# Optimization experiments

Measured on AMD Instinct MI355X. Metric: run time of the kernel, lower is better.

## Reference

```python
import jax, jax.numpy as jnp
import numpy as np

B, H, S, Q = 32768, 896, 448, 256  # batch, hidden, split=hidden//2, quantisation


def setup_inputs() -> dict:
    key = jax.random.key(0)
    ks = jax.random.split(key, 16)
    sc = 0.02
    return {
        'prev_y': jax.random.uniform(ks[0], (B, 2), jnp.float32) * 2.0 - 1.0,
        'prev_hidden': jax.random.normal(ks[1], (B, H), jnp.float32),
        'current_coarse': jax.random.uniform(ks[2], (B, 1), jnp.float32) * 2.0 - 1.0,
        'W_R': jax.random.normal(ks[3], (H, 3 * H), jnp.float32) * sc,
        'W_Ic': jax.random.normal(ks[4], (2, 3 * S), jnp.float32) * sc,
        'W_If': jax.random.normal(ks[5], (3, 3 * S), jnp.float32) * sc,
        'W_O1': jax.random.normal(ks[6], (S, S), jnp.float32) * sc,
        'b_O1': jnp.zeros((S,), jnp.float32),
        'W_O2': jax.random.normal(ks[7], (S, Q), jnp.float32) * sc,
        'b_O2': jnp.zeros((Q,), jnp.float32),
        'W_O3': jax.random.normal(ks[8], (S, S), jnp.float32) * sc,
        'b_O3': jnp.zeros((S,), jnp.float32),
        'W_O4': jax.random.normal(ks[9], (S, Q), jnp.float32) * sc,
        'b_O4': jnp.zeros((Q,), jnp.float32),
        'bias_u': jnp.zeros((H,), jnp.float32),
        'bias_r': jnp.zeros((H,), jnp.float32),
        'bias_e': jnp.zeros((H,), jnp.float32),
    }


def reference(prev_y, prev_hidden, current_coarse, W_R, W_Ic, W_If,
              W_O1, b_O1, W_O2, b_O2, W_O3, b_O3, W_O4, b_O4,
              bias_u, bias_r, bias_e):
    # recurrent projection of previous hidden state: [B, 3H]
    R_u, R_r, R_e = jnp.split(prev_hidden @ W_R, 3, axis=1)
    # coarse-half input projection from (prev_coarse, prev_fine): [B, 3S]
    I_cu, I_cr, I_ce = jnp.split(prev_y @ W_Ic, 3, axis=1)
    # fine-half input projection from (prev_coarse, prev_fine, current_coarse): [B, 3S]
    fine_in = jnp.concatenate([prev_y, current_coarse], axis=1)
    I_fu, I_fr, I_fe = jnp.split(fine_in @ W_If, 3, axis=1)
    I_u = jnp.concatenate([I_cu, I_fu], axis=1)
    I_r = jnp.concatenate([I_cr, I_fr], axis=1)
    I_e = jnp.concatenate([I_ce, I_fe], axis=1)
    u = jax.nn.sigmoid(R_u + I_u + bias_u)
    r = jax.nn.sigmoid(R_r + I_r + bias_r)
    e = jnp.tanh(r * R_e + I_e + bias_e)
    hidden = u * prev_hidden + (1.0 - u) * e
    h_c, h_f = jnp.split(hidden, 2, axis=1)
    out_coarse = jax.nn.relu(h_c @ W_O1 + b_O1) @ W_O2 + b_O2
    out_fine = jax.nn.relu(h_f @ W_O3 + b_O3) @ W_O4 + b_O4
    return out_coarse, out_fine, hidden
```

## Files before the change

kernel.cpp:

```cpp
#include <hip/hip_runtime.h>


typedef unsigned short u16;
typedef unsigned int u32;
typedef __attribute__((ext_vector_type(8))) short bf16x8;
typedef __attribute__((ext_vector_type(4))) float f32x4;

#define GAS __attribute__((address_space(1)))
#define LAS __attribute__((address_space(3)))

__device__ __forceinline__ u16 f2b(float f) {
  union { float f; u32 i; } v; v.f = f;
  return (u16)((v.i + 0x7fffu + ((v.i >> 16) & 1u)) >> 16);
}

__device__ __forceinline__ void gl_lds(const u16* g, u16* l) {
  __builtin_amdgcn_global_load_lds((const GAS void*)g, (LAS void*)l, 16, 0, 0);
}

__global__ void cvt_f32_bf16(const float* __restrict__ in, u16* __restrict__ outp) {
  const size_t i = ((size_t)blockIdx.x * 256 + threadIdx.x) * 4;
  const float4 v = *(const float4*)&in[i];
  ushort4 o;
  o.x = f2b(v.x); o.y = f2b(v.y); o.z = f2b(v.z); o.w = f2b(v.w);
  *(ushort4*)&outp[i] = o;
}

__device__ __forceinline__ void transpose_body(const float* __restrict__ in,
                                               u16* __restrict__ outp,
                                               int R, int C, int c0, int r0) {
  __shared__ u16 t[32][33];
  const int x = threadIdx.x, y = threadIdx.y;
  #pragma unroll
  for (int i = 0; i < 32; i += 8)
    t[y + i][x] = f2b(in[(size_t)(r0 + y + i) * C + (c0 + x)]);
  __syncthreads();
  #pragma unroll
  for (int i = 0; i < 32; i += 8)
    outp[(size_t)(c0 + y + i) * R + (r0 + x)] = t[x][y + i];
}

__global__ void transpose_f32_bf16(const float* __restrict__ in, u16* __restrict__ outp,
                                   int R, int C) {
  transpose_body(in, outp, R, C, blockIdx.x * 32, blockIdx.y * 32);
}

__global__ void transpose_wo(const float* __restrict__ w1, const float* __restrict__ w2,
                             const float* __restrict__ w3, const float* __restrict__ w4,
                             u16* __restrict__ o1, u16* __restrict__ o2,
                             u16* __restrict__ o3, u16* __restrict__ o4) {
  const int z = blockIdx.z;
  const float* in = (z == 0) ? w1 : (z == 1) ? w2 : (z == 2) ? w3 : w4;
  u16* outp = (z == 0) ? o1 : (z == 1) ? o2 : (z == 2) ? o3 : o4;
  const int C = (z & 1) ? 256 : 448;
  const int c0 = blockIdx.x * 32;
  if (c0 >= C) return;
  transpose_body(in, outp, 448, C, c0, blockIdx.y * 32);
}

__device__ __forceinline__ void gemm_tile_k(const u16* __restrict__ A, int lda,
                                            const u16* __restrict__ BT, int ldb,
                                            int K, u16* Al, u16* Bl,
                                            int wave, int lane, f32x4 (&acc)[4][4]) {
  const int wm = wave & 1, wn = wave >> 1;
  const int q = lane >> 4, l16 = lane & 15;
  const int qs = q ^ ((l16 >> 1) & 3);
  const int sr = lane >> 2;
  const int sc = ((lane & 3) ^ ((lane >> 3) & 3)) * 8;
  for (int k0 = 0; k0 < K; k0 += 32) {
    #pragma unroll
    for (int i = 0; i < 2; ++i) {
      const int rr = wave * 32 + i * 16;
      gl_lds(A + (size_t)(rr + sr) * lda + (k0 + sc), &Al[rr * 32]);
      gl_lds(BT + (size_t)(rr + sr) * ldb + (k0 + sc), &Bl[rr * 32]);
    }
    __syncthreads();
    bf16x8 af[4], bfr[4];
    #pragma unroll
    for (int t = 0; t < 4; ++t) {
      af[t]  = *(const bf16x8*)&Al[(wm * 64 + t * 16 + l16) * 32 + qs * 8];
      bfr[t] = *(const bf16x8*)&Bl[(wn * 64 + t * 16 + l16) * 32 + qs * 8];
    }
    #pragma unroll
    for (int mt = 0; mt < 4; ++mt)
      #pragma unroll
      for (int nt = 0; nt < 4; ++nt)
        acc[mt][nt] = __builtin_amdgcn_mfma_f32_16x16x32_bf16(af[mt], bfr[nt],
                                                              acc[mt][nt], 0, 0, 0);
    __syncthreads();
  }
}

__device__ __forceinline__ void zero_acc(f32x4 (&acc)[4][4]) {
  const f32x4 z = {0.f, 0.f, 0.f, 0.f};
  #pragma unroll
  for (int mt = 0; mt < 4; ++mt)
    #pragma unroll
    for (int nt = 0; nt < 4; ++nt)
      acc[mt][nt] = z;
}

__global__ __launch_bounds__(1024, 4)
void gate_kernel(const u16* __restrict__ phb, const u16* __restrict__ wrt,
                 const float* __restrict__ phf,
                 const float* __restrict__ y2, const float* __restrict__ cc,
                 const float* __restrict__ wic, const float* __restrict__ wif,
                 const float* __restrict__ bu, const float* __restrict__ br,
                 const float* __restrict__ be,
                 float* __restrict__ houtf, u16* __restrict__ hb) {
  __shared__ u16 Sl[3][16384];
  __shared__ float rowy[3 * 128];
  const int tid = threadIdx.x;
  const int lane = tid & 63, wave = tid >> 6;
  const int f = blockIdx.x;
  const int xcd = f & 7, l = f >> 3;
  const int m0 = (xcd * 32 + l / 7) * 128;
  const int j0 = (l % 7) * 128;
  if (tid < 128) {
    const int r = m0 + tid;
    rowy[tid]       = y2[2 * r];
    rowy[128 + tid] = y2[2 * r + 1];
    rowy[256 + tid] = cc[r];
    asm volatile("s_waitcnt lgkmcnt(0)" ::: "memory");
  }
  const int wm = wave & 3, wn = wave >> 2;
  const int q = lane >> 4, l16 = lane & 15;
  const int qs = q ^ ((l16 >> 1) & 3);
  const int sr = lane >> 2;
  const int sc = ((lane & 3) ^ ((lane >> 3) & 3)) * 8;

  const int u0 = 2 * wave, u1 = u0 + 1;
  const u16* g0; const u16* g1; int lo0, lo1;
  if (u0 < 8) { g0 = phb + (size_t)(m0 + u0 * 16 + sr) * 896 + sc; lo0 = u0 * 512; }
  else { const int nn = u0 - 8, jj = nn / 3, s = nn % 3;
         g0 = wrt + (size_t)(s * 896 + j0 + jj * 16 + sr) * 896 + sc;
         lo0 = 4096 + nn * 512; }
  if (u1 < 8) { g1 = phb + (size_t)(m0 + u1 * 16 + sr) * 896 + sc; lo1 = u1 * 512; }
  else { const int nn = u1 - 8, jj = nn / 3, s = nn % 3;
         g1 = wrt + (size_t)(s * 896 + j0 + jj * 16 + sr) * 896 + sc;
         lo1 = 4096 + nn * 512; }

  f32x4 acc[2][3][2];
  {
    const f32x4 z = {0.f, 0.f, 0.f, 0.f};
    #pragma unroll
    for (int a = 0; a < 2; ++a)
      #pragma unroll
      for (int s = 0; s < 3; ++s)
        #pragma unroll
        for (int m = 0; m < 2; ++m)
          acc[a][s][m] = z;
  }

  auto stage = [&](int t_) {
    const int b_ = t_ % 3;
    const int k_ = t_ * 32;
    gl_lds(g0 + k_, &Sl[b_][lo0]);
    gl_lds(g1 + k_, &Sl[b_][lo1]);
  };

  stage(0);
  stage(1);
  for (int t = 0; t < 28; ++t) {
    if (t < 27) asm volatile("s_waitcnt vmcnt(2)" ::: "memory");
    else        asm volatile("s_waitcnt vmcnt(0)" ::: "memory");
    __builtin_amdgcn_s_barrier();
    __builtin_amdgcn_sched_barrier(0);
    const u16* Sb = Sl[t % 3];
    bf16x8 af[2];
    #pragma unroll
    for (int mt = 0; mt < 2; ++mt)
      af[mt] = *(const bf16x8*)&Sb[(wm * 32 + mt * 16 + l16) * 32 + qs * 8];
    #pragma unroll
    for (int jj2 = 0; jj2 < 2; ++jj2)
      #pragma unroll
      for (int s = 0; s < 3; ++s) {
        const int nn = (2 * wn + jj2) * 3 + s;
        const bf16x8 bf_ = *(const bf16x8*)&Sb[4096 + nn * 512 + l16 * 32 + qs * 8];
        #pragma unroll
        for (int mt = 0; mt < 2; ++mt)
          acc[jj2][s][mt] = __builtin_amdgcn_mfma_f32_16x16x32_bf16(
              af[mt], bf_, acc[jj2][s][mt], 0, 0, 0);
      }
    if (t + 2 < 28) stage(t + 2);
  }

  #pragma unroll
  for (int jj2 = 0; jj2 < 2; ++jj2) {
    const int j = j0 + (2 * wn + jj2) * 16 + l16;
    float wu0, wu1, wu2, wr0, wr1, wr2, we0, we1, we2;
    if (j < 448) {
      wu0 = wic[j];       wu1 = wic[1344 + j];       wu2 = 0.f;
      wr0 = wic[448 + j]; wr1 = wic[1792 + j];       wr2 = 0.f;
      we0 = wic[896 + j]; we1 = wic[2240 + j];       we2 = 0.f;
    } else {
      const int jf = j - 448;
      wu0 = wif[jf];       wu1 = wif[1344 + jf]; wu2 = wif[2688 + jf];
      wr0 = wif[448 + jf]; wr1 = wif[1792 + jf]; wr2 = wif[3136 + jf];
      we0 = wif[896 + jf]; we1 = wif[2240 + jf]; we2 = wif[3584 + jf];
    }
    const float bju = bu[j], bjr = br[j], bje = be[j];
    #pragma unroll
    for (int mt = 0; mt < 2; ++mt) {
      const int rl = wm * 32 + mt * 16 + q * 4;
      #pragma unroll
      for (int i = 0; i < 4; ++i) {
        const float y0 = rowy[rl + i], y1 = rowy[128 + rl + i], yc = rowy[256 + rl + i];
        const float gu = acc[jj2][0][mt][i] + y0 * wu0 + y1 * wu1 + yc * wu2 + bju;
        const float gr = acc[jj2][1][mt][i] + y0 * wr0 + y1 * wr1 + yc * wr2 + bjr;
        const float uu = 1.f / (1.f + __expf(-gu));
        const float rg = 1.f / (1.f + __expf(-gr));
        const float ev = tanhf(rg * acc[jj2][2][mt][i] +
                               y0 * we0 + y1 * we1 + yc * we2 + bje);
        const size_t grow = (size_t)(m0 + rl + i);
        const float phv = phf[grow * 896 + j];
        const float h = uu * phv + (1.f - uu) * ev;
        houtf[grow * 896 + j] = h;
        hb[grow * 896 + j] = f2b(h);
      }
    }
  }
}

__global__ __launch_bounds__(256, 2)
void stage1_kernel(const u16* __restrict__ hb, const u16* __restrict__ w1t,
                   const u16* __restrict__ w3t, const float* __restrict__ b1,
                   const float* __restrict__ b3, u16* __restrict__ tc,
                   u16* __restrict__ tf) {
  __shared__ u16 Al[128 * 32];
  __shared__ u16 Bl[128 * 32];
  const int tid = threadIdx.x, lane = tid & 63, wave = tid >> 6;
  const int f = blockIdx.x;
  const int xcd = f & 7, l = f >> 3;
  const int mz = xcd * 64 + (l >> 2);
  const int z = mz >> 8;
  const int m0 = (mz & 255) * 128, n0 = (l & 3) * 128;
  const u16* A = hb + (size_t)m0 * 896 + z * 448;
  const u16* BT = (z ? w3t : w1t) + (size_t)n0 * 448;
  const float* bias = z ? b3 : b1;
  u16* T = z ? tf : tc;
  const int wm = wave & 1, wn = wave >> 1, q = lane >> 4, l16 = lane & 15;
  f32x4 acc[4][4];
  zero_acc(acc);
  gemm_tile_k(A, 896, BT, 448, 448, Al, Bl, wave, lane, acc);
  #pragma unroll
  for (int nt = 0; nt < 4; ++nt) {
    const int j = n0 + wn * 64 + nt * 16 + l16;
    if (j < 448) {
      const float bv = bias[j];
      #pragma unroll
      for (int mt = 0; mt < 4; ++mt)
        #pragma unroll
        for (int i = 0; i < 4; ++i) {
          const size_t row = (size_t)(m0 + wm * 64 + mt * 16 + q * 4 + i);
          T[row * 448 + j] = f2b(fmaxf(acc[mt][nt][i] + bv, 0.f));
        }
    }
  }
}

__global__ __launch_bounds__(256, 2)
void stage2_kernel(const u16* __restrict__ tc, const u16* __restrict__ tf,
                   const u16* __restrict__ w2t, const u16* __restrict__ w4t,
                   const float* __restrict__ b2_, const float* __restrict__ b4,
                   float* __restrict__ out) {
  __shared__ u16 Al[128 * 32];
  __shared__ u16 Bl[128 * 32];
  const int tid = threadIdx.x, lane = tid & 63, wave = tid >> 6;
  const int f = blockIdx.x;
  const int xcd = f & 7, l = f >> 3;
  const int mz = xcd * 64 + (l >> 1);
  const int z = mz >> 8;
  const int m0 = (mz & 255) * 128, n0 = (l & 1) * 128;
  const u16* A = (z ? tf : tc) + (size_t)m0 * 448;
  const u16* BT = (z ? w4t : w2t) + (size_t)n0 * 448;
  const float* bias = z ? b4 : b2_;
  float* O = out + (size_t)z * 32768 * 256;
  const int wm = wave & 1, wn = wave >> 1, q = lane >> 4, l16 = lane & 15;
  f32x4 acc[4][4];
  zero_acc(acc);
  gemm_tile_k(A, 448, BT, 448, 448, Al, Bl, wave, lane, acc);
  #pragma unroll
  for (int nt = 0; nt < 4; ++nt) {
    const int j = n0 + wn * 64 + nt * 16 + l16;
    const float bv = bias[j];
    #pragma unroll
    for (int mt = 0; mt < 4; ++mt)
      #pragma unroll
      for (int i = 0; i < 4; ++i) {
        const size_t row = (size_t)(m0 + wm * 64 + mt * 16 + q * 4 + i);
        O[row * 256 + j] = acc[mt][nt][i] + bv;
      }
  }
}

extern "C" void kernel_launch(void* const* d_in, const int* in_sizes, int n_in,
                              void* d_out, int out_size, void* d_ws, size_t ws_size,
                              hipStream_t stream) {
  const float* y2   = (const float*)d_in[0];
  const float* ph   = (const float*)d_in[1];
  const float* cc   = (const float*)d_in[2];
  const float* W_R  = (const float*)d_in[3];
  const float* W_Ic = (const float*)d_in[4];
  const float* W_If = (const float*)d_in[5];
  const float* W_O1 = (const float*)d_in[6];
  const float* b_O1 = (const float*)d_in[7];
  const float* W_O2 = (const float*)d_in[8];
  const float* b_O2 = (const float*)d_in[9];
  const float* W_O3 = (const float*)d_in[10];
  const float* b_O3 = (const float*)d_in[11];
  const float* W_O4 = (const float*)d_in[12];
  const float* b_O4 = (const float*)d_in[13];
  const float* bu   = (const float*)d_in[14];
  const float* br   = (const float*)d_in[15];
  const float* be   = (const float*)d_in[16];
  float* out = (float*)d_out;
  u16* ws  = (u16*)d_ws;

  u16* WRT = ws;
  u16* W1T = WRT + (size_t)2688 * 896;
  u16* W2T = W1T + 448 * 448;
  u16* W3T = W2T + 256 * 448;
  u16* W4T = W3T + 448 * 448;
  u16* phb = W4T + 256 * 448;
  u16* hb  = phb + (size_t)32768 * 896;
  u16* Tc  = phb;
  u16* Tf  = phb + (size_t)32768 * 448;
  float* hidf = out + (size_t)2 * 32768 * 256;

  dim3 tb(32, 8);
  cvt_f32_bf16<<<28672, 256, 0, stream>>>(ph, phb);
  transpose_f32_bf16<<<dim3(2688 / 32, 896 / 32), tb, 0, stream>>>(W_R, WRT, 896, 2688);
  transpose_wo<<<dim3(14, 14, 4), tb, 0, stream>>>(W_O1, W_O2, W_O3, W_O4,
                                                   W1T, W2T, W3T, W4T);

  gate_kernel<<<1792, 1024, 0, stream>>>(phb, WRT, ph, y2, cc, W_Ic, W_If,
                                         bu, br, be, hidf, hb);
  stage1_kernel<<<2048, 256, 0, stream>>>(hb, W1T, W3T, b_O1, b_O3, Tc, Tf);
  stage2_kernel<<<1024, 256, 0, stream>>>(Tc, Tf, W2T, W4T, b_O2, b_O4, out);
}
```

Measured before the change: 632.7 us.

## Load A fragments directly from global, enlarge gate tile, triple-buffer MLP GEMMs

The gate kernel now covers 256 rows per block instead of 128, with half as many blocks. Each wave loads its A (hidden-state) fragments straight from global memory into registers, and only the W_R tiles are staged in LDS, at K-steps of 64 with triple buffering. The two MLP stage kernels replace their synchronous double-barrier GEMM loop with the same scheme: A read directly from global memory and B triple-buffered in LDS through async global-to-LDS loads. This is meant to cut LDS traffic and barriers, and to give more MFMA work per staged byte. The cost is uncoalesced direct global A loads and higher register pressure, with occupancy bounds changed to 3.

```diff
diff --git a/kernel.cpp b/kernel.cpp
--- a/kernel.cpp
+++ b/kernel.cpp
@@ -58,49 +58,7 @@
   transpose_body(in, outp, 448, C, c0, blockIdx.y * 32);
 }
 
-__device__ __forceinline__ void gemm_tile_k(const u16* __restrict__ A, int lda,
-                                            const u16* __restrict__ BT, int ldb,
-                                            int K, u16* Al, u16* Bl,
-                                            int wave, int lane, f32x4 (&acc)[4][4]) {
-  const int wm = wave & 1, wn = wave >> 1;
-  const int q = lane >> 4, l16 = lane & 15;
-  const int qs = q ^ ((l16 >> 1) & 3);
-  const int sr = lane >> 2;
-  const int sc = ((lane & 3) ^ ((lane >> 3) & 3)) * 8;
-  for (int k0 = 0; k0 < K; k0 += 32) {
-    #pragma unroll
-    for (int i = 0; i < 2; ++i) {
-      const int rr = wave * 32 + i * 16;
-      gl_lds(A + (size_t)(rr + sr) * lda + (k0 + sc), &Al[rr * 32]);
-      gl_lds(BT + (size_t)(rr + sr) * ldb + (k0 + sc), &Bl[rr * 32]);
-    }
-    __syncthreads();
-    bf16x8 af[4], bfr[4];
-    #pragma unroll
-    for (int t = 0; t < 4; ++t) {
-      af[t]  = *(const bf16x8*)&Al[(wm * 64 + t * 16 + l16) * 32 + qs * 8];
-      bfr[t] = *(const bf16x8*)&Bl[(wn * 64 + t * 16 + l16) * 32 + qs * 8];
-    }
-    #pragma unroll
-    for (int mt = 0; mt < 4; ++mt)
-      #pragma unroll
-      for (int nt = 0; nt < 4; ++nt)
-        acc[mt][nt] = __builtin_amdgcn_mfma_f32_16x16x32_bf16(af[mt], bfr[nt],
-                                                              acc[mt][nt], 0, 0, 0);
-    __syncthreads();
-  }
-}
-
-__device__ __forceinline__ void zero_acc(f32x4 (&acc)[4][4]) {
-  const f32x4 z = {0.f, 0.f, 0.f, 0.f};
-  #pragma unroll
-  for (int mt = 0; mt < 4; ++mt)
-    #pragma unroll
-    for (int nt = 0; nt < 4; ++nt)
-      acc[mt][nt] = z;
-}
-
-__global__ __launch_bounds__(1024, 4)
+__global__ __launch_bounds__(1024, 3)
 void gate_kernel(const u16* __restrict__ phb, const u16* __restrict__ wrt,
                  const float* __restrict__ phf,
                  const float* __restrict__ y2, const float* __restrict__ cc,
@@ -108,19 +66,19 @@
                  const float* __restrict__ bu, const float* __restrict__ br,
                  const float* __restrict__ be,
                  float* __restrict__ houtf, u16* __restrict__ hb) {
-  __shared__ u16 Sl[3][16384];
-  __shared__ float rowy[3 * 128];
+  __shared__ u16 Bl[3][24576];
+  __shared__ float rowy[3 * 256];
   const int tid = threadIdx.x;
   const int lane = tid & 63, wave = tid >> 6;
   const int f = blockIdx.x;
   const int xcd = f & 7, l = f >> 3;
-  const int m0 = (xcd * 32 + l / 7) * 128;
+  const int m0 = (xcd * 16 + l / 7) * 256;
   const int j0 = (l % 7) * 128;
-  if (tid < 128) {
+  if (tid < 256) {
     const int r = m0 + tid;
     rowy[tid]       = y2[2 * r];
-    rowy[128 + tid] = y2[2 * r + 1];
-    rowy[256 + tid] = cc[r];
+    rowy[256 + tid] = y2[2 * r + 1];
+    rowy[512 + tid] = cc[r];
     asm volatile("s_waitcnt lgkmcnt(0)" ::: "memory");
   }
   const int wm = wave & 3, wn = wave >> 2;
@@ -129,18 +87,18 @@
   const int sr = lane >> 2;
   const int sc = ((lane & 3) ^ ((lane >> 3) & 3)) * 8;
 
-  const int u0 = 2 * wave, u1 = u0 + 1;
-  const u16* g0; const u16* g1; int lo0, lo1;
-  if (u0 < 8) { g0 = phb + (size_t)(m0 + u0 * 16 + sr) * 896 + sc; lo0 = u0 * 512; }
-  else { const int nn = u0 - 8, jj = nn / 3, s = nn % 3;
-         g0 = wrt + (size_t)(s * 896 + j0 + jj * 16 + sr) * 896 + sc;
-         lo0 = 4096 + nn * 512; }
-  if (u1 < 8) { g1 = phb + (size_t)(m0 + u1 * 16 + sr) * 896 + sc; lo1 = u1 * 512; }
-  else { const int nn = u1 - 8, jj = nn / 3, s = nn % 3;
-         g1 = wrt + (size_t)(s * 896 + j0 + jj * 16 + sr) * 896 + sc;
-         lo1 = 4096 + nn * 512; }
-
-  f32x4 acc[2][3][2];
+  const u16* ag = phb + (size_t)(m0 + wm * 64 + l16) * 896 + q * 8;
+
+  const u16* gs[3]; int lo[3];
+  #pragma unroll
+  for (int i = 0; i < 3; ++i) {
+    const int u = 3 * wave + i, nn = u >> 1, kh = u & 1;
+    const int s = nn % 3, jj = nn / 3;
+    gs[i] = wrt + (size_t)(s * 896 + j0 + jj * 16 + sr) * 896 + (kh * 32 + sc);
+    lo[i] = u * 512;
+  }
+
+  f32x4 acc[2][3][4];
   {
     const f32x4 z = {0.f, 0.f, 0.f, 0.f};
     #pragma unroll
@@ -148,41 +106,48 @@
       #pragma unroll
       for (int s = 0; s < 3; ++s)
         #pragma unroll
-        for (int m = 0; m < 2; ++m)
+        for (int m = 0; m < 4; ++m)
           acc[a][s][m] = z;
   }
 
   auto stage = [&](int t_) {
-    const int b_ = t_ % 3;
-    const int k_ = t_ * 32;
-    gl_lds(g0 + k_, &Sl[b_][lo0]);
-    gl_lds(g1 + k_, &Sl[b_][lo1]);
+    u16* base = &Bl[t_ % 3][0];
+    const int koff = t_ * 64;
+    #pragma unroll
+    for (int i = 0; i < 3; ++i) gl_lds(gs[i] + koff, base + lo[i]);
   };
 
-  stage(0);
-  stage(1);
-  for (int t = 0; t < 28; ++t) {
-    if (t < 27) asm volatile("s_waitcnt vmcnt(2)" ::: "memory");
-    else        asm volatile("s_waitcnt vmcnt(0)" ::: "memory");
+  stage(0); stage(1);
+  for (int t = 0; t < 14; ++t) {
+    if (t == 0) asm volatile("s_waitcnt vmcnt(3)" ::: "memory");
+    else        asm volatile("s_waitcnt vmcnt(11)" ::: "memory");
     __builtin_amdgcn_s_barrier();
     __builtin_amdgcn_sched_barrier(0);
-    const u16* Sb = Sl[t % 3];
-    bf16x8 af[2];
-    #pragma unroll
-    for (int mt = 0; mt < 2; ++mt)
-      af[mt] = *(const bf16x8*)&Sb[(wm * 32 + mt * 16 + l16) * 32 + qs * 8];
-    #pragma unroll
-    for (int jj2 = 0; jj2 < 2; ++jj2)
-      #pragma unroll
-      for (int s = 0; s < 3; ++s) {
-        const int nn = (2 * wn + jj2) * 3 + s;
-        const bf16x8 bf_ = *(const bf16x8*)&Sb[4096 + nn * 512 + l16 * 32 + qs * 8];
-        #pragma unroll
-        for (int mt = 0; mt < 2; ++mt)
-          acc[jj2][s][mt] = __builtin_amdgcn_mfma_f32_16x16x32_bf16(
-              af[mt], bf_, acc[jj2][s][mt], 0, 0, 0);
+    bf16x8 af[2][4];
+    #pragma unroll
+    for (int kh = 0; kh < 2; ++kh)
+      #pragma unroll
+      for (int mt = 0; mt < 4; ++mt)
+        af[kh][mt] = *(const bf16x8*)(ag + (size_t)mt * 16 * 896 + t * 64 + kh * 32);
+    stage(t + 2 < 13 ? t + 2 : 13);
+    const u16* Sb = &Bl[t % 3][0];
+    #pragma unroll
+    for (int kh = 0; kh < 2; ++kh)
+      #pragma unroll
+      for (int jj2 = 0; jj2 < 2; ++jj2) {
+        bf16x8 bf_[3];
+        #pragma unroll
+        for (int s = 0; s < 3; ++s) {
+          const int nn = (2 * wn + jj2) * 3 + s;
+          bf_[s] = *(const bf16x8*)&Sb[nn * 1024 + kh * 512 + l16 * 32 + qs * 8];
+        }
+        #pragma unroll
+        for (int s = 0; s < 3; ++s)
+          #pragma unroll
+          for (int mt = 0; mt < 4; ++mt)
+            acc[jj2][s][mt] = __builtin_amdgcn_mfma_f32_16x16x32_bf16(
+                af[kh][mt], bf_[s], acc[jj2][s][mt], 0, 0, 0);
       }
-    if (t + 2 < 28) stage(t + 2);
   }
 
   #pragma unroll
@@ -201,11 +166,11 @@
     }
     const float bju = bu[j], bjr = br[j], bje = be[j];
     #pragma unroll
-    for (int mt = 0; mt < 2; ++mt) {
-      const int rl = wm * 32 + mt * 16 + q * 4;
+    for (int mt = 0; mt < 4; ++mt) {
+      const int rl = wm * 64 + mt * 16 + q * 4;
       #pragma unroll
       for (int i = 0; i < 4; ++i) {
-        const float y0 = rowy[rl + i], y1 = rowy[128 + rl + i], yc = rowy[256 + rl + i];
+        const float y0 = rowy[rl + i], y1 = rowy[256 + rl + i], yc = rowy[512 + rl + i];
         const float gu = acc[jj2][0][mt][i] + y0 * wu0 + y1 * wu1 + yc * wu2 + bju;
         const float gr = acc[jj2][1][mt][i] + y0 * wr0 + y1 * wr1 + yc * wr2 + bjr;
         const float uu = 1.f / (1.f + __expf(-gu));
@@ -222,13 +187,74 @@
   }
 }
 
-__global__ __launch_bounds__(256, 2)
+__device__ __forceinline__ void mlp_gemm(const u16* __restrict__ A, int lda,
+                                         const u16* __restrict__ BT, int ldb,
+                                         u16 (&Bl)[3][8192],
+                                         int wave, int lane, f32x4 (&acc)[4][4]) {
+  const int wm = wave & 1, wn = wave >> 1;
+  const int q = lane >> 4, l16 = lane & 15;
+  const int qs = q ^ ((l16 >> 1) & 3);
+  const int sr = lane >> 2;
+  const int sc = ((lane & 3) ^ ((lane >> 3) & 3)) * 8;
+  const u16* ag = A + (size_t)(wm * 64 + l16) * lda + q * 8;
+  const u16* gs[4]; int lo[4];
+  #pragma unroll
+  for (int i = 0; i < 4; ++i) {
+    const int u = 4 * wave + i, ntile = u >> 1, kh = u & 1;
+    gs[i] = BT + (size_t)(ntile * 16 + sr) * ldb + (kh * 32 + sc);
+    lo[i] = u * 512;
+  }
+  auto stage = [&](int t_) {
+    u16* base = &Bl[t_ % 3][0];
+    const int koff = t_ * 64;
+    #pragma unroll
+    for (int i = 0; i < 4; ++i) gl_lds(gs[i] + koff, base + lo[i]);
+  };
+  stage(0); stage(1);
+  for (int t = 0; t < 7; ++t) {
+    if (t == 0) asm volatile("s_waitcnt vmcnt(4)" ::: "memory");
+    else        asm volatile("s_waitcnt vmcnt(12)" ::: "memory");
+    __builtin_amdgcn_s_barrier();
+    __builtin_amdgcn_sched_barrier(0);
+    bf16x8 af[2][4];
+    #pragma unroll
+    for (int kh = 0; kh < 2; ++kh)
+      #pragma unroll
+      for (int mt = 0; mt < 4; ++mt)
+        af[kh][mt] = *(const bf16x8*)(ag + (size_t)mt * 16 * lda + t * 64 + kh * 32);
+    stage(t + 2 < 6 ? t + 2 : 6);
+    const u16* Sb = &Bl[t % 3][0];
+    #pragma unroll
+    for (int kh = 0; kh < 2; ++kh) {
+      bf16x8 bf_[4];
+      #pragma unroll
+      for (int nf = 0; nf < 4; ++nf)
+        bf_[nf] = *(const bf16x8*)&Sb[(wn * 4 + nf) * 1024 + kh * 512 + l16 * 32 + qs * 8];
+      #pragma unroll
+      for (int nf = 0; nf < 4; ++nf)
+        #pragma unroll
+        for (int mt = 0; mt < 4; ++mt)
+          acc[mt][nf] = __builtin_amdgcn_mfma_f32_16x16x32_bf16(
+              af[kh][mt], bf_[nf], acc[mt][nf], 0, 0, 0);
+    }
+  }
+}
+
+__device__ __forceinline__ void zero_acc(f32x4 (&acc)[4][4]) {
+  const f32x4 z = {0.f, 0.f, 0.f, 0.f};
+  #pragma unroll
+  for (int mt = 0; mt < 4; ++mt)
+    #pragma unroll
+    for (int nt = 0; nt < 4; ++nt)
+      acc[mt][nt] = z;
+}
+
+__global__ __launch_bounds__(256, 3)
 void stage1_kernel(const u16* __restrict__ hb, const u16* __restrict__ w1t,
                    const u16* __restrict__ w3t, const float* __restrict__ b1,
                    const float* __restrict__ b3, u16* __restrict__ tc,
                    u16* __restrict__ tf) {
-  __shared__ u16 Al[128 * 32];
-  __shared__ u16 Bl[128 * 32];
+  __shared__ u16 Bl[3][8192];
   const int tid = threadIdx.x, lane = tid & 63, wave = tid >> 6;
   const int f = blockIdx.x;
   const int xcd = f & 7, l = f >> 3;
@@ -242,10 +268,10 @@
   const int wm = wave & 1, wn = wave >> 1, q = lane >> 4, l16 = lane & 15;
   f32x4 acc[4][4];
   zero_acc(acc);
-  gemm_tile_k(A, 896, BT, 448, 448, Al, Bl, wave, lane, acc);
-  #pragma unroll
-  for (int nt = 0; nt < 4; ++nt) {
-    const int j = n0 + wn * 64 + nt * 16 + l16;
+  mlp_gemm(A, 896, BT, 448, Bl, wave, lane, acc);
+  #pragma unroll
+  for (int nf = 0; nf < 4; ++nf) {
+    const int j = n0 + wn * 64 + nf * 16 + l16;
     if (j < 448) {
       const float bv = bias[j];
       #pragma unroll
@@ -253,19 +279,18 @@
         #pragma unroll
         for (int i = 0; i < 4; ++i) {
           const size_t row = (size_t)(m0 + wm * 64 + mt * 16 + q * 4 + i);
-          T[row * 448 + j] = f2b(fmaxf(acc[mt][nt][i] + bv, 0.f));
+          T[row * 448 + j] = f2b(fmaxf(acc[mt][nf][i] + bv, 0.f));
         }
     }
   }
 }
 
-__global__ __launch_bounds__(256, 2)
+__global__ __launch_bounds__(256, 3)
 void stage2_kernel(const u16* __restrict__ tc, const u16* __restrict__ tf,
                    const u16* __restrict__ w2t, const u16* __restrict__ w4t,
                    const float* __restrict__ b2_, const float* __restrict__ b4,
                    float* __restrict__ out) {
-  __shared__ u16 Al[128 * 32];
-  __shared__ u16 Bl[128 * 32];
+  __shared__ u16 Bl[3][8192];
   const int tid = threadIdx.x, lane = tid & 63, wave = tid >> 6;
   const int f = blockIdx.x;
   const int xcd = f & 7, l = f >> 3;
@@ -279,17 +304,17 @@
   const int wm = wave & 1, wn = wave >> 1, q = lane >> 4, l16 = lane & 15;
   f32x4 acc[4][4];
   zero_acc(acc);
-  gemm_tile_k(A, 448, BT, 448, 448, Al, Bl, wave, lane, acc);
-  #pragma unroll
-  for (int nt = 0; nt < 4; ++nt) {
-    const int j = n0 + wn * 64 + nt * 16 + l16;
+  mlp_gemm(A, 448, BT, 448, Bl, wave, lane, acc);
+  #pragma unroll
+  for (int nf = 0; nf < 4; ++nf) {
+    const int j = n0 + wn * 64 + nf * 16 + l16;
     const float bv = bias[j];
     #pragma unroll
     for (int mt = 0; mt < 4; ++mt)
       #pragma unroll
       for (int i = 0; i < 4; ++i) {
         const size_t row = (size_t)(m0 + wm * 64 + mt * 16 + q * 4 + i);
-        O[row * 256 + j] = acc[mt][nt][i] + bv;
+        O[row * 256 + j] = acc[mt][nf][i] + bv;
       }
   }
 }
@@ -334,8 +359,8 @@
   transpose_wo<<<dim3(14, 14, 4), tb, 0, stream>>>(W_O1, W_O2, W_O3, W_O4,
                                                    W1T, W2T, W3T, W4T);
 
-  gate_kernel<<<1792, 1024, 0, stream>>>(phb, WRT, ph, y2, cc, W_Ic, W_If,
-                                         bu, br, be, hidf, hb);
+  gate_kernel<<<896, 1024, 0, stream>>>(phb, WRT, ph, y2, cc, W_Ic, W_If,
+                                        bu, br, be, hidf, hb);
   stage1_kernel<<<2048, 256, 0, stream>>>(hb, W1T, W3T, b_O1, b_O3, Tc, Tf);
   stage2_kernel<<<1024, 256, 0, stream>>>(Tc, Tf, W2T, W4T, b_O2, b_O4, out);
 }
```

Result: slower. 1.344 ms (+112.5%).

## Triple-buffer stage GEMMs with async LDS loads and 8-wave blocks

Applied to the files above, without the earlier changes.

Replaces the single-buffered GEMM loop in both output-MLP stages with a 3-stage LDS ring buffer. Global-to-LDS loads are issued two K-steps ahead and waited on with explicit vmcnt counters, so there is one barrier per step instead of two. Blocks grow from 4 to 8 waves, each wave computing a 64x32 sub-tile instead of 64x64, which halves per-thread accumulators to help occupancy. The cost is more LDS per block (48 KB) and reliance on hand-written waitcnt ordering, which hard-codes K=448.

```diff
diff --git a/kernel.cpp b/kernel.cpp
--- a/kernel.cpp
+++ b/kernel.cpp
@@ -56,48 +56,6 @@
   const int c0 = blockIdx.x * 32;
   if (c0 >= C) return;
   transpose_body(in, outp, 448, C, c0, blockIdx.y * 32);
-}
-
-__device__ __forceinline__ void gemm_tile_k(const u16* __restrict__ A, int lda,
-                                            const u16* __restrict__ BT, int ldb,
-                                            int K, u16* Al, u16* Bl,
-                                            int wave, int lane, f32x4 (&acc)[4][4]) {
-  const int wm = wave & 1, wn = wave >> 1;
-  const int q = lane >> 4, l16 = lane & 15;
-  const int qs = q ^ ((l16 >> 1) & 3);
-  const int sr = lane >> 2;
-  const int sc = ((lane & 3) ^ ((lane >> 3) & 3)) * 8;
-  for (int k0 = 0; k0 < K; k0 += 32) {
-    #pragma unroll
-    for (int i = 0; i < 2; ++i) {
-      const int rr = wave * 32 + i * 16;
-      gl_lds(A + (size_t)(rr + sr) * lda + (k0 + sc), &Al[rr * 32]);
-      gl_lds(BT + (size_t)(rr + sr) * ldb + (k0 + sc), &Bl[rr * 32]);
-    }
-    __syncthreads();
-    bf16x8 af[4], bfr[4];
-    #pragma unroll
-    for (int t = 0; t < 4; ++t) {
-      af[t]  = *(const bf16x8*)&Al[(wm * 64 + t * 16 + l16) * 32 + qs * 8];
-      bfr[t] = *(const bf16x8*)&Bl[(wn * 64 + t * 16 + l16) * 32 + qs * 8];
-    }
-    #pragma unroll
-    for (int mt = 0; mt < 4; ++mt)
-      #pragma unroll
-      for (int nt = 0; nt < 4; ++nt)
-        acc[mt][nt] = __builtin_amdgcn_mfma_f32_16x16x32_bf16(af[mt], bfr[nt],
-                                                              acc[mt][nt], 0, 0, 0);
-    __syncthreads();
-  }
-}
-
-__device__ __forceinline__ void zero_acc(f32x4 (&acc)[4][4]) {
-  const f32x4 z = {0.f, 0.f, 0.f, 0.f};
-  #pragma unroll
-  for (int mt = 0; mt < 4; ++mt)
-    #pragma unroll
-    for (int nt = 0; nt < 4; ++nt)
-      acc[mt][nt] = z;
 }
 
 __global__ __launch_bounds__(1024, 4)
@@ -222,13 +180,64 @@
   }
 }
 
-__global__ __launch_bounds__(256, 2)
+__device__ __forceinline__ void stage_gemm(const u16* __restrict__ A, int lda,
+                                           const u16* __restrict__ BT, int ldb,
+                                           u16 (&Bl)[3][8192],
+                                           int wave, int lane, f32x4 (&acc)[4][2]) {
+  const int wm = wave & 1, wn = wave >> 1;
+  const int q = lane >> 4, l16 = lane & 15;
+  const int qs = q ^ ((l16 >> 1) & 3);
+  const int sr = lane >> 2;
+  const int sc = ((lane & 3) ^ ((lane >> 3) & 3)) * 8;
+  const u16* gs0; const u16* gs1; int lo0, lo1;
+  {
+    const int u = 2 * wave;
+    gs0 = (u < 8) ? A + (size_t)(u * 16 + sr) * lda + sc
+                  : BT + (size_t)((u - 8) * 16 + sr) * ldb + sc;
+    lo0 = u * 512;
+  }
+  {
+    const int u = 2 * wave + 1;
+    gs1 = (u < 8) ? A + (size_t)(u * 16 + sr) * lda + sc
+                  : BT + (size_t)((u - 8) * 16 + sr) * ldb + sc;
+    lo1 = u * 512;
+  }
+  auto stage = [&](int t_) {
+    u16* base = &Bl[t_ % 3][0];
+    const int koff = t_ * 32;
+    gl_lds(gs0 + koff, base + lo0);
+    gl_lds(gs1 + koff, base + lo1);
+  };
+  stage(0); stage(1);
+  for (int t = 0; t < 14; ++t) {
+    if (t < 13) asm volatile("s_waitcnt vmcnt(2)" ::: "memory");
+    else        asm volatile("s_waitcnt vmcnt(0)" ::: "memory");
+    __builtin_amdgcn_s_barrier();
+    __builtin_amdgcn_sched_barrier(0);
+    const u16* Sb = &Bl[t % 3][0];
+    bf16x8 af[4], bfr[2];
+    #pragma unroll
+    for (int mt = 0; mt < 4; ++mt)
+      af[mt] = *(const bf16x8*)&Sb[(wm * 64 + mt * 16 + l16) * 32 + qs * 8];
+    #pragma unroll
+    for (int nt = 0; nt < 2; ++nt)
+      bfr[nt] = *(const bf16x8*)&Sb[4096 + (wn * 32 + nt * 16 + l16) * 32 + qs * 8];
+    #pragma unroll
+    for (int mt = 0; mt < 4; ++mt)
+      #pragma unroll
+      for (int nt = 0; nt < 2; ++nt)
+        acc[mt][nt] = __builtin_amdgcn_mfma_f32_16x16x32_bf16(af[mt], bfr[nt],
+                                                              acc[mt][nt], 0, 0, 0);
+    if (t + 2 < 14) stage(t + 2);
+  }
+}
+
+__global__ __launch_bounds__(512, 4)
 void stage1_kernel(const u16* __restrict__ hb, const u16* __restrict__ w1t,
                    const u16* __restrict__ w3t, const float* __restrict__ b1,
                    const float* __restrict__ b3, u16* __restrict__ tc,
                    u16* __restrict__ tf) {
-  __shared__ u16 Al[128 * 32];
-  __shared__ u16 Bl[128 * 32];
+  __shared__ u16 Bl[3][8192];
   const int tid = threadIdx.x, lane = tid & 63, wave = tid >> 6;
   const int f = blockIdx.x;
   const int xcd = f & 7, l = f >> 3;
@@ -240,12 +249,19 @@
   const float* bias = z ? b3 : b1;
   u16* T = z ? tf : tc;
   const int wm = wave & 1, wn = wave >> 1, q = lane >> 4, l16 = lane & 15;
-  f32x4 acc[4][4];
-  zero_acc(acc);
-  gemm_tile_k(A, 896, BT, 448, 448, Al, Bl, wave, lane, acc);
-  #pragma unroll
-  for (int nt = 0; nt < 4; ++nt) {
-    const int j = n0 + wn * 64 + nt * 16 + l16;
+  f32x4 acc[4][2];
+  {
+    const f32x4 zz = {0.f, 0.f, 0.f, 0.f};
+    #pragma unroll
+    for (int mt = 0; mt < 4; ++mt)
+      #pragma unroll
+      for (int nt = 0; nt < 2; ++nt)
+        acc[mt][nt] = zz;
+  }
+  stage_gemm(A, 896, BT, 448, Bl, wave, lane, acc);
+  #pragma unroll
+  for (int nt = 0; nt < 2; ++nt) {
+    const int j = n0 + wn * 32 + nt * 16 + l16;
     if (j < 448) {
       const float bv = bias[j];
       #pragma unroll
@@ -259,13 +275,12 @@
   }
 }
 
-__global__ __launch_bounds__(256, 2)
+__global__ __launch_bounds__(512, 4)
 void stage2_kernel(const u16* __restrict__ tc, const u16* __restrict__ tf,
                    const u16* __restrict__ w2t, const u16* __restrict__ w4t,
                    const float* __restrict__ b2_, const float* __restrict__ b4,
                    float* __restrict__ out) {
-  __shared__ u16 Al[128 * 32];
-  __shared__ u16 Bl[128 * 32];
+  __shared__ u16 Bl[3][8192];
   const int tid = threadIdx.x, lane = tid & 63, wave = tid >> 6;
   const int f = blockIdx.x;
   const int xcd = f & 7, l = f >> 3;
@@ -277,12 +292,19 @@
   const float* bias = z ? b4 : b2_;
   float* O = out + (size_t)z * 32768 * 256;
   const int wm = wave & 1, wn = wave >> 1, q = lane >> 4, l16 = lane & 15;
-  f32x4 acc[4][4];
-  zero_acc(acc);
-  gemm_tile_k(A, 448, BT, 448, 448, Al, Bl, wave, lane, acc);
-  #pragma unroll
-  for (int nt = 0; nt < 4; ++nt) {
-    const int j = n0 + wn * 64 + nt * 16 + l16;
+  f32x4 acc[4][2];
+  {
+    const f32x4 zz = {0.f, 0.f, 0.f, 0.f};
+    #pragma unroll
+    for (int mt = 0; mt < 4; ++mt)
+      #pragma unroll
+      for (int nt = 0; nt < 2; ++nt)
+        acc[mt][nt] = zz;
+  }
+  stage_gemm(A, 448, BT, 448, Bl, wave, lane, acc);
+  #pragma unroll
+  for (int nt = 0; nt < 2; ++nt) {
+    const int j = n0 + wn * 32 + nt * 16 + l16;
     const float bv = bias[j];
     #pragma unroll
     for (int mt = 0; mt < 4; ++mt)
@@ -336,6 +358,6 @@
 
   gate_kernel<<<1792, 1024, 0, stream>>>(phb, WRT, ph, y2, cc, W_Ic, W_If,
                                          bu, br, be, hidf, hb);
-  stage1_kernel<<<2048, 256, 0, stream>>>(hb, W1T, W3T, b_O1, b_O3, Tc, Tf);
-  stage2_kernel<<<1024, 256, 0, stream>>>(Tc, Tf, W2T, W4T, b_O2, b_O4, out);
-}
+  stage1_kernel<<<2048, 512, 0, stream>>>(hb, W1T, W3T, b_O1, b_O3, Tc, Tf);
+  stage2_kernel<<<1024, 512, 0, stream>>>(Tc, Tf, W2T, W4T, b_O2, b_O4, out);
+}
```

Result: faster. 610.3 us (-3.5%).
